# Performance work log

Measured on AMD Instinct MI355X. Metric: run time of the kernel, lower is better.

The kernel has to match this reference:

```python
import jax, jax.numpy as jnp
import numpy as np

N_P, N_A, D, H, E = 200000, 100000, 64, 32, 1000000


def setup_inputs() -> dict:
    key = jax.random.key(0)
    ks = jax.random.split(key, 32)
    inp = {}
    inp["x_paper"] = jax.random.normal(ks[0], (N_P, D), jnp.float32)
    inp["x_author"] = jax.random.normal(ks[1], (N_A, D), jnp.float32)
    inp["cites_src"] = jax.random.randint(ks[2], (E,), 0, N_P, jnp.int32)
    inp["cites_dst"] = jax.random.randint(ks[3], (E,), 0, N_P, jnp.int32)
    inp["writes_src"] = jax.random.randint(ks[4], (E,), 0, N_A, jnp.int32)
    inp["writes_dst"] = jax.random.randint(ks[5], (E,), 0, N_P, jnp.int32)
    inp["rev_src"] = jax.random.randint(ks[6], (E,), 0, N_P, jnp.int32)
    inp["rev_dst"] = jax.random.randint(ks[7], (E,), 0, N_A, jnp.int32)
    # per-relation SAGEConv params; layer 1: D->H, layer 2: H->H
    i = 8
    for layer, din in ((1, D), (2, H)):
        for rel in ("cites", "writes", "rev"):
            inp[f"W{layer}l_{rel}"] = 0.1 * jax.random.normal(ks[i], (din, H), jnp.float32); i += 1
            inp[f"W{layer}r_{rel}"] = 0.1 * jax.random.normal(ks[i], (din, H), jnp.float32); i += 1
            inp[f"b{layer}_{rel}"] = 0.01 * jax.random.normal(ks[i], (H,), jnp.float32); i += 1
    return inp


def _sage(x_src, x_dst, src, dst, Wl, Wr, b, n_dst):
    # PyG SAGEConv (aggr='mean'): lin_l(mean of source msgs) + lin_r(x_dst) + bias
    msg = x_src[src]                                              # [E, d] gather
    s = jax.ops.segment_sum(msg, dst, num_segments=n_dst)         # [n_dst, d]
    cnt = jax.ops.segment_sum(jnp.ones((src.shape[0],), x_src.dtype), dst, num_segments=n_dst)
    mean = s / jnp.maximum(cnt, 1.0)[:, None]
    return mean @ Wl + x_dst @ Wr + b


def reference(x_paper, x_author, cites_src, cites_dst, writes_src, writes_dst,
              rev_src, rev_dst,
              W1l_cites, W1r_cites, b1_cites, W1l_writes, W1r_writes, b1_writes,
              W1l_rev, W1r_rev, b1_rev,
              W2l_cites, W2r_cites, b2_cites, W2l_writes, W2r_writes, b2_writes,
              W2l_rev, W2r_rev, b2_rev):
    n_p, n_a = x_paper.shape[0], x_author.shape[0]
    # layer 1 (to_hetero sums relation outputs per dst node type), then relu
    p1 = jax.nn.relu(
        _sage(x_paper, x_paper, cites_src, cites_dst, W1l_cites, W1r_cites, b1_cites, n_p)
        + _sage(x_author, x_paper, writes_src, writes_dst, W1l_writes, W1r_writes, b1_writes, n_p))
    a1 = jax.nn.relu(
        _sage(x_paper, x_author, rev_src, rev_dst, W1l_rev, W1r_rev, b1_rev, n_a))
    # layer 2, return 'paper' output (no activation)
    p2 = (_sage(p1, p1, cites_src, cites_dst, W2l_cites, W2r_cites, b2_cites, n_p)
          + _sage(a1, p1, writes_src, writes_dst, W2l_writes, W2r_writes, b2_writes, n_p))
    return p2
```

## Files before the change

### kernel.cpp

```cpp
#include <hip/hip_runtime.h>

typedef unsigned short u16;
typedef unsigned int   u32;
typedef unsigned char  u8;
typedef __attribute__((ext_vector_type(8))) short bf16x8;
typedef __attribute__((ext_vector_type(4))) float f32x4;

#define N_P 200000
#define N_A 100000
#define DD  64
#define HH  32
#define NE  1000000
#define NBP 782
#define NBA 391
#define NB4K 245
#define NCB 196
#define P4CAP 8192
#define NB_P16 12500
#define NB_A16 6250
#define NB4K3 735

__device__ inline float bf2f(u16 u) { return __uint_as_float(((u32)u) << 16); }
__device__ inline u16 f2bf(float f) {
    u32 u = __float_as_uint(f);
    u += 0x7fffu + ((u >> 16) & 1u);
    return (u16)(u >> 16);
}
__device__ inline float lo_f(u32 m) { return __uint_as_float(m << 16); }
__device__ inline float hi_f(u32 m) { return __uint_as_float(m & 0xffff0000u); }
__device__ inline u32 cvtpk(float a, float b) {
    u32 r;
    asm("v_cvt_pk_bf16_f32 %0, %1, %2" : "=v"(r) : "v"(a), "v"(b));
    return r;
}

__device__ inline void gseg_dual(
    const u16* __restrict__ yA, const int* __restrict__ bkA, int s0, int e0,
    const u16* __restrict__ yB, const int* __restrict__ bkB, int s1, int e1,
    int lane, float& axo, float& ayo, float& bxo, float& byo) {
    float ax = 0.f, ay = 0.f, bx = 0.f, by = 0.f;
    int lastA = min(max(e0 - 1, s0), NE - 1);
    int lastB = min(max(e1 - 1, s1), NE - 1);
    for (int j0 = s0, j1 = s1; (j0 < e0) || (j1 < e1); j0 += 8, j1 += 8) {
        int ia[8], ib[8];
#pragma unroll
        for (int i = 0; i < 8; ++i) ia[i] = bkA[min(j0 + i, lastA)];
#pragma unroll
        for (int i = 0; i < 8; ++i) ib[i] = bkB[min(j1 + i, lastB)];
        u32 ma[8], mb[8];
#pragma unroll
        for (int i = 0; i < 8; ++i)
            ma[i] = *(const u32*)(yA + (size_t)(u32)ia[i] + lane * 2);
#pragma unroll
        for (int i = 0; i < 8; ++i)
            mb[i] = *(const u32*)(yB + (size_t)(u32)ib[i] + lane * 2);
#pragma unroll
        for (int i = 0; i < 8; ++i) {
            u32 va = (j0 + i < e0) ? ma[i] : 0u;
            ax += lo_f(va); ay += hi_f(va);
        }
#pragma unroll
        for (int i = 0; i < 8; ++i) {
            u32 vb = (j1 + i < e1) ? mb[i] : 0u;
            bx += lo_f(vb); by += hi_f(vb);
        }
    }
    axo = ax; ayo = ay; bxo = bx; byo = by;
}

__global__ __launch_bounds__(256) void p1_hist_k(
    const int* __restrict__ cd, const int* __restrict__ wd, const int* __restrict__ rd,
    int* __restrict__ gsizes) {
    int rel = blockIdx.y;
    const int* dst; int shift;
    if (rel == 0)      { dst = cd; shift = 10; }
    else if (rel == 1) { dst = wd; shift = 10; }
    else               { dst = rd; shift = 9;  }
    __shared__ int cnt[256];
    int t = threadIdx.x;
    cnt[t] = 0;
    __syncthreads();
    int e0 = blockIdx.x * 4096;
    if (e0 + 4096 <= NE) {
        const int4* dv = (const int4*)(dst + e0);
#pragma unroll
        for (int i = 0; i < 4; ++i) {
            int4 v = dv[i * 256 + t];
            atomicAdd(&cnt[v.x >> shift], 1);
            atomicAdd(&cnt[v.y >> shift], 1);
            atomicAdd(&cnt[v.z >> shift], 1);
            atomicAdd(&cnt[v.w >> shift], 1);
        }
    } else {
#pragma unroll
        for (int i = 0; i < 16; ++i) {
            int e = e0 + i * 256 + t;
            if (e < NE) atomicAdd(&cnt[dst[e] >> shift], 1);
        }
    }
    __syncthreads();
    if (t < NCB && cnt[t]) atomicAdd(&gsizes[rel * NCB + t], cnt[t]);
}

__global__ __launch_bounds__(256) void p2_scan_k(
    const int* __restrict__ gsizes, int* __restrict__ bases, int* __restrict__ gcur) {
    __shared__ int lds[256];
    int t = threadIdx.x;
    for (int rel = 0; rel < 3; ++rel) {
        int v = (t < NCB) ? gsizes[rel * NCB + t] : 0;
        lds[t] = v; __syncthreads();
#pragma unroll
        for (int o = 1; o < 256; o <<= 1) {
            int x = (t >= o) ? lds[t - o] : 0;
            __syncthreads();
            lds[t] += x;
            __syncthreads();
        }
        int ex = lds[t] - v;
        if (t < NCB) { bases[rel * NCB + t] = ex; gcur[rel * NCB + t] = ex; }
        __syncthreads();
    }
}

__global__ __launch_bounds__(256) void p3t1_k(
    const int* __restrict__ cs, const int* __restrict__ cd,
    const int* __restrict__ ws_, const int* __restrict__ wd,
    const int* __restrict__ rs, const int* __restrict__ rd,
    int* __restrict__ gcur,
    u32* __restrict__ pr_c, u32* __restrict__ pr_w, u32* __restrict__ pr_r,
    const float* __restrict__ xp, const float* __restrict__ xa,
    const u16* __restrict__ wt1h, const u16* __restrict__ wt1l,
    const float* __restrict__ b1s, const float* __restrict__ b1r,
    u16* __restrict__ y_pc, u16* __restrict__ y_pr, u16* __restrict__ y_aw,
    u16* __restrict__ hb_p, u16* __restrict__ hb_a) {
    __shared__ float smem[256 * 34];
    int t = threadIdx.x;
    if (blockIdx.x < NB4K3) {
        u32* sbuf  = (u32*)smem;
        int* cnt   = (int*)(smem + 4096);
        int* sc    = (int*)(smem + 4352);
        int* lcur  = (int*)(smem + 4608);
        int* gbase = (int*)(smem + 4864);
        u8*  bb    = (u8*)(smem + 5120);
        int rel = blockIdx.x / NB4K;
        int blk = blockIdx.x - rel * NB4K;
        const int *src, *dst; int shift; u32* out;
        if (rel == 0)      { src = cs;  dst = cd; shift = 10; out = pr_c; }
        else if (rel == 1) { src = ws_; dst = wd; shift = 10; out = pr_w; }
        else               { src = rs;  dst = rd; shift = 9;  out = pr_r; }
        cnt[t] = 0;
        __syncthreads();
        int e0 = blk * 4096;
        int myd[16], mys[16];
        if (e0 + 4096 <= NE) {
            const int4* dv = (const int4*)(dst + e0);
            const int4* sv = (const int4*)(src + e0);
#pragma unroll
            for (int i = 0; i < 4; ++i) {
                int4 v = dv[i * 256 + t];
                int4 s = sv[i * 256 + t];
                myd[4 * i] = v.x; myd[4 * i + 1] = v.y; myd[4 * i + 2] = v.z; myd[4 * i + 3] = v.w;
                mys[4 * i] = s.x; mys[4 * i + 1] = s.y; mys[4 * i + 2] = s.z; mys[4 * i + 3] = s.w;
                atomicAdd(&cnt[v.x >> shift], 1);
                atomicAdd(&cnt[v.y >> shift], 1);
                atomicAdd(&cnt[v.z >> shift], 1);
                atomicAdd(&cnt[v.w >> shift], 1);
            }
        } else {
#pragma unroll
            for (int i = 0; i < 4; ++i) {
#pragma unroll
                for (int c = 0; c < 4; ++c) {
                    int e = e0 + (i * 256 + t) * 4 + c;
                    int idx = 4 * i + c;
                    if (e < NE) {
                        myd[idx] = dst[e]; mys[idx] = src[e];
                        atomicAdd(&cnt[myd[idx] >> shift], 1);
                    } else { myd[idx] = -1; mys[idx] = 0; }
                }
            }
        }
        __syncthreads();
        int v = cnt[t];
        sc[t] = v; __syncthreads();
#pragma unroll
        for (int o = 1; o < 256; o <<= 1) {
            int x = (t >= o) ? sc[t - o] : 0;
            __syncthreads();
            sc[t] += x;
            __syncthreads();
        }
        int ex = sc[t] - v;
        __syncthreads();
        sc[t] = ex;
        lcur[t] = ex;
        if (t < NCB) gbase[t] = atomicAdd(&gcur[rel * NCB + t], cnt[t]);
        __syncthreads();
#pragma unroll
        for (int i = 0; i < 16; ++i) {
            if (myd[i] >= 0) {
                int d = myd[i];
                int cb = d >> shift;
                u32 dloc = (u32)(d - (cb << shift));
                u32 pk = (dloc << 18) | (u32)mys[i];
                int p = atomicAdd(&lcur[cb], 1);
                sbuf[p] = pk;
                bb[p] = (u8)cb;
            }
        }
        __syncthreads();
        int nvalid = min(4096, NE - e0);
        for (int i = t; i < nvalid; i += 256) {
            int cb = bb[i];
            out[gbase[cb] + (i - sc[cb])] = sbuf[i];
        }
    } else {
        float* Cs = smem;
        int w = t >> 6, l = t & 63;
        int lm = l & 15, lk = l >> 4;
        int bx = blockIdx.x - NB4K3;
        bool paper = bx < NBP;
        int row0 = (paper ? bx : bx - NBP) * 256;
        const float* x = paper ? xp : xa;
        int NROW = paper ? N_P : N_A;
        int nv = min(256, NROW - row0);
        bf16x8 xh[4][2], xl[4][2];
#pragma unroll
        for (int i = 0; i < 4; ++i) {
            int rowg = min(row0 + w * 64 + i * 16 + lm, NROW - 1);
            const float* rp = x + (size_t)rowg * DD + lk * 8;
#pragma unroll
            for (int kc = 0; kc < 2; ++kc) {
                float4 a = *(const float4*)(rp + kc * 32);
                float4 b = *(const float4*)(rp + kc * 32 + 4);
                float f[8] = {a.x, a.y, a.z, a.w, b.x, b.y, b.z, b.w};
                union { u32 u[4]; bf16x8 v; } H, L;
#pragma unroll
                for (int j = 0; j < 4; ++j) {
                    u32 u0 = __float_as_uint(f[2 * j]);
                    u32 u1 = __float_as_uint(f[2 * j + 1]);
                    u32 m0 = u0 & 0xffff0000u;
                    u32 m1 = u1 & 0xffff0000u;
                    H.u[j] = (u0 >> 16) | m1;
                    float l0 = f[2 * j]     - __uint_as_float(m0);
                    float l1 = f[2 * j + 1] - __uint_as_float(m1);
                    L.u[j] = cvtpk(l0, l1);
                }
                xh[i][kc] = H.v; xl[i][kc] = L.v;
            }
        }
        int nw = paper ? 3 : 2;
#pragma unroll 1
        for (int iw = 0; iw < nw; ++iw) {
            int mat = paper ? iw : (3 + iw);
            const u16* Wh = wt1h + mat * 2048;
            const u16* Wl = wt1l + mat * 2048;
            bf16x8 Bh[2][2], Bl[2][2];
#pragma unroll
            for (int ct = 0; ct < 2; ++ct)
#pragma unroll
                for (int kc = 0; kc < 2; ++kc) {
                    int off = (ct * 16 + lm) * 64 + kc * 32 + lk * 8;
                    Bh[ct][kc] = *(const bf16x8*)(Wh + off);
                    Bl[ct][kc] = *(const bf16x8*)(Wl + off);
                }
            float bv[2] = {0.f, 0.f};
            if (paper && iw == 2)  { bv[0] = b1s[lm]; bv[1] = b1s[16 + lm]; }
            if (!paper && iw == 1) { bv[0] = b1r[lm]; bv[1] = b1r[16 + lm]; }
#pragma unroll
            for (int i = 0; i < 4; ++i) {
#pragma unroll
                for (int ct = 0; ct < 2; ++ct) {
                    f32x4 acc = {bv[ct], bv[ct], bv[ct], bv[ct]};
                    acc = __builtin_amdgcn_mfma_f32_16x16x32_bf16(xh[i][0], Bh[ct][0], acc, 0, 0, 0);
                    acc = __builtin_amdgcn_mfma_f32_16x16x32_bf16(xh[i][1], Bh[ct][1], acc, 0, 0, 0);
                    acc = __builtin_amdgcn_mfma_f32_16x16x32_bf16(xl[i][0], Bh[ct][0], acc, 0, 0, 0);
                    acc = __builtin_amdgcn_mfma_f32_16x16x32_bf16(xl[i][1], Bh[ct][1], acc, 0, 0, 0);
                    acc = __builtin_amdgcn_mfma_f32_16x16x32_bf16(xh[i][0], Bl[ct][0], acc, 0, 0, 0);
                    acc = __builtin_amdgcn_mfma_f32_16x16x32_bf16(xh[i][1], Bl[ct][1], acc, 0, 0, 0);
                    int rbase = w * 64 + i * 16 + lk * 4;
#pragma unroll
                    for (int r = 0; r < 4; ++r)
                        Cs[(rbase + r) * 34 + ct * 16 + lm] = acc[r];
                }
            }
            asm volatile("s_waitcnt lgkmcnt(0)" ::: "memory");
            u16* outp;
            if (paper) outp = (iw == 0) ? y_pc : (iw == 1) ? y_pr : hb_p;
            else       outp = (iw == 0) ? y_aw : hb_a;
            u32* g = (u32*)(outp + (size_t)row0 * HH);
#pragma unroll
            for (int p = 0; p < 4; ++p) {
                int j = p * 64 + l;
                int rl = w * 64 + (j >> 2);
                if (rl < nv) {
                    const float* q = Cs + rl * 34 + (j & 3) * 8;
                    u32 o[4];
#pragma unroll
                    for (int jj = 0; jj < 4; ++jj)
                        o[jj] = cvtpk(q[2 * jj], q[2 * jj + 1]);
                    *(uint4*)(g + ((size_t)w * 256 + j) * 4) = make_uint4(o[0], o[1], o[2], o[3]);
                }
            }
            asm volatile("" ::: "memory");
        }
    }
}

__global__ __launch_bounds__(256) void p4_sort_k(
    const int* __restrict__ bases, const int* __restrict__ gsizes,
    const u32* __restrict__ pr_c, const u32* __restrict__ pr_w, const u32* __restrict__ pr_r,
    int* __restrict__ bkt_c, int* __restrict__ bkt_w, int* __restrict__ bkt_r,
    int* __restrict__ st_c, int* __restrict__ st_w, int* __restrict__ st_r) {
    int rel = blockIdx.y;
    const u32* pr; int* bkt; int* st; int width, n;
    if (rel == 0)      { pr = pr_c; bkt = bkt_c; st = st_c; width = 1024; n = N_P; }
    else if (rel == 1) { pr = pr_w; bkt = bkt_w; st = st_w; width = 1024; n = N_P; }
    else               { pr = pr_r; bkt = bkt_r; st = st_r; width = 512;  n = N_A; }
    __shared__ u32 sin[P4CAP];
    __shared__ int cnt[1024], sc2[1024], tmp[256];
    int t = threadIdx.x;
    int b = blockIdx.x;
    int base = bases[rel * NCB + b];
    int size = min(gsizes[rel * NCB + b], P4CAP);
    int d0 = b * width;
    int nd = min(width, n - d0);
    if (nd <= 0) return;
#pragma unroll
    for (int j = t; j < 1024; j += 256) cnt[j] = 0;
    __syncthreads();
    for (int i = t; i < size; i += 256) {
        u32 pk = pr[base + i];
        sin[i] = pk;
        atomicAdd(&cnt[pk >> 18], 1);
    }
    __syncthreads();
    int j0 = 4 * t;
    int c0 = cnt[j0], c1 = cnt[j0 + 1], c2 = cnt[j0 + 2], c3 = cnt[j0 + 3];
    int tot = c0 + c1 + c2 + c3;
    tmp[t] = tot; __syncthreads();
#pragma unroll
    for (int o = 1; o < 256; o <<= 1) {
        int x = (t >= o) ? tmp[t - o] : 0;
        __syncthreads();
        tmp[t] += x;
        __syncthreads();
    }
    int pre = tmp[t] - tot;
    sc2[j0] = pre;
    sc2[j0 + 1] = pre + c0;
    sc2[j0 + 2] = pre + c0 + c1;
    sc2[j0 + 3] = pre + c0 + c1 + c2;
    __syncthreads();
    for (int j = t; j < nd; j += 256) st[d0 + j] = base + sc2[j];
#pragma unroll
    for (int j = t; j < 1024; j += 256) cnt[j] = 0;
    __syncthreads();
    for (int i = t; i < size; i += 256) {
        u32 pk = sin[i];
        int dl = (int)(pk >> 18);
        int pos = sc2[dl] + atomicAdd(&cnt[dl], 1);
        bkt[base + pos] = (int)((pk & 0x3FFFFu) * HH);
    }
}

__global__ __launch_bounds__(256) void prep_w_k(
    const float* __restrict__ W1lc, const float* __restrict__ W1lr,
    const float* __restrict__ W1rc, const float* __restrict__ W1rw,
    const float* __restrict__ W1lw, const float* __restrict__ W1rr,
    const float* __restrict__ W2lc, const float* __restrict__ W2rc,
    const float* __restrict__ W2rw, const float* __restrict__ W2lw,
    const float* __restrict__ b1c, const float* __restrict__ b1w,
    const float* __restrict__ b2c, const float* __restrict__ b2w,
    u16* __restrict__ wt1h, u16* __restrict__ wt1l,
    u16* __restrict__ wt2h, u16* __restrict__ wt2l,
    float* __restrict__ b1s, float* __restrict__ b2s,
    int* __restrict__ gsizes) {
    int m = blockIdx.x, t = threadIdx.x;
    if (m == 0) {
        for (int e = t; e < 3 * NCB; e += 256) gsizes[e] = 0;
    }
    if (m < 5) {
        const float *A = nullptr, *B = nullptr;
        if (m == 0) A = W1lc;
        else if (m == 1) A = W1lr;
        else if (m == 2) { A = W1rc; B = W1rw; }
        else if (m == 3) A = W1lw;
        else A = W1rr;
        for (int e = t; e < 2048; e += 256) {
            int k = e >> 5, n = e & 31;
            float v = A[e] + (B ? B[e] : 0.f);
            u16 h = f2bf(v);
            u16 lw = f2bf(v - bf2f(h));
            wt1h[m * 2048 + n * 64 + k] = h;
            wt1l[m * 2048 + n * 64 + k] = lw;
        }
        if (m == 2 && t < HH) b1s[t] = b1c[t] + b1w[t];
    } else {
        int mm = m - 5;
        const float *A = nullptr, *B = nullptr;
        if (mm == 0) A = W2lc;
        else if (mm == 1) { A = W2rc; B = W2rw; }
        else A = W2lw;
        for (int e = t; e < 1024; e += 256) {
            int k = e >> 5, n = e & 31;
            float v = A[e] + (B ? B[e] : 0.f);
            u16 h = f2bf(v);
            u16 lw = f2bf(v - bf2f(h));
            wt2h[mm * 1024 + n * 32 + k] = h;
            wt2l[mm * 1024 + n * 32 + k] = lw;
        }
        if (mm == 1 && t < HH) b2s[t] = b2c[t] + b2w[t];
    }
}

__global__ __launch_bounds__(256) void agg1_k(
    const u16* __restrict__ y_pc, const u16* __restrict__ y_aw,
    const u16* __restrict__ y_pr,
    const int* __restrict__ st_c, const int* __restrict__ bkt_c,
    const int* __restrict__ st_w, const int* __restrict__ bkt_w,
    const int* __restrict__ st_r, const int* __restrict__ bkt_r,
    u32* __restrict__ hb_p, u32* __restrict__ hb_a) {
    int t = threadIdx.x, g = t >> 4, lane = t & 15;
    if (blockIdx.x < NB_P16) {
        int row = blockIdx.x * 16 + g;
        u32 self = hb_p[(size_t)row * (HH / 2) + lane];
        int s0 = st_c[row];
        int e0 = (row == N_P - 1) ? NE : st_c[row + 1];
        int s1 = st_w[row];
        int e1 = (row == N_P - 1) ? NE : st_w[row + 1];
        float cx, cy, wx, wy;
        gseg_dual(y_pc, bkt_c, s0, e0, y_aw, bkt_w, s1, e1, lane, cx, cy, wx, wy);
        int d0 = e0 - s0, d1 = e1 - s1;
        float iv0 = 1.0f / (float)(d0 < 1 ? 1 : d0);
        float iv1 = 1.0f / (float)(d1 < 1 ? 1 : d1);
        float ax = cx * iv0 + wx * iv1 + lo_f(self);
        float ay = cy * iv0 + wy * iv1 + hi_f(self);
        hb_p[(size_t)row * (HH / 2) + lane] = cvtpk(ax, ay);
    } else {
        int row = (blockIdx.x - NB_P16) * 16 + g;
        u32 self = hb_a[(size_t)row * (HH / 2) + lane];
        int s = st_r[row];
        int e = (row == N_A - 1) ? NE : st_r[row + 1];
        int mid = (s + e) >> 1;
        float ax0, ay0, ax1, ay1;
        gseg_dual(y_pr, bkt_r, s, mid, y_pr, bkt_r, mid, e, lane, ax0, ay0, ax1, ay1);
        int dg = e - s;
        float iv = 1.0f / (float)(dg < 1 ? 1 : dg);
        float ax = (ax0 + ax1) * iv + lo_f(self);
        float ay = (ay0 + ay1) * iv + hi_f(self);
        hb_a[(size_t)row * (HH / 2) + lane] = cvtpk(ax, ay);
    }
}

__global__ __launch_bounds__(256) void t2_k(
    const u32* __restrict__ hb_p, const u32* __restrict__ hb_a,
    const u16* __restrict__ wt2h, const u16* __restrict__ wt2l,
    const float* __restrict__ b2s,
    u16* __restrict__ z_p, u16* __restrict__ z_a, float* __restrict__ hp2) {
    __shared__ float Cs[256 * 34];
    int t = threadIdx.x, w = t >> 6, l = t & 63;
    int lm = l & 15, lk = l >> 4;
    bool paper = blockIdx.x < NBP;
    int row0 = (paper ? blockIdx.x : blockIdx.x - NBP) * 256;
    const u32* hb = paper ? hb_p : hb_a;
    int NROW = paper ? N_P : N_A;
    int nv = min(256, NROW - row0);
    bf16x8 af[4];
#pragma unroll
    for (int i = 0; i < 4; ++i) {
        int rowg = min(row0 + w * 64 + i * 16 + lm, NROW - 1);
        uint4 q = *(const uint4*)(hb + (size_t)rowg * (HH / 2) + lk * 4);
        u32 qq[4] = {q.x, q.y, q.z, q.w};
        union { u32 u[4]; bf16x8 v; } A;
#pragma unroll
        for (int j = 0; j < 4; ++j) {
            u32 m = ((qq[j] & 0x80008000u) >> 15) * 0xFFFFu;
            A.u[j] = qq[j] & ~m;
        }
        af[i] = A.v;
    }
    int nw = paper ? 2 : 1;
#pragma unroll 1
    for (int iw = 0; iw < nw; ++iw) {
        int mat = paper ? iw : 2;
        const u16* Wh = wt2h + mat * 1024;
        const u16* Wl = wt2l + mat * 1024;
        bf16x8 Bh[2], Bl[2];
#pragma unroll
        for (int ct = 0; ct < 2; ++ct) {
            int off = (ct * 16 + lm) * 32 + lk * 8;
            Bh[ct] = *(const bf16x8*)(Wh + off);
            Bl[ct] = *(const bf16x8*)(Wl + off);
        }
        float bv[2] = {0.f, 0.f};
        if (paper && iw == 1) { bv[0] = b2s[lm]; bv[1] = b2s[16 + lm]; }
#pragma unroll
        for (int i = 0; i < 4; ++i) {
#pragma unroll
            for (int ct = 0; ct < 2; ++ct) {
                f32x4 acc = {bv[ct], bv[ct], bv[ct], bv[ct]};
                acc = __builtin_amdgcn_mfma_f32_16x16x32_bf16(af[i], Bh[ct], acc, 0, 0, 0);
                acc = __builtin_amdgcn_mfma_f32_16x16x32_bf16(af[i], Bl[ct], acc, 0, 0, 0);
                int rbase = w * 64 + i * 16 + lk * 4;
#pragma unroll
                for (int r = 0; r < 4; ++r)
                    Cs[(rbase + r) * 34 + ct * 16 + lm] = acc[r];
            }
        }
        asm volatile("s_waitcnt lgkmcnt(0)" ::: "memory");
        if (paper && iw == 1) {
            float* gf = hp2 + (size_t)row0 * HH;
#pragma unroll
            for (int p = 0; p < 8; ++p) {
                int j = p * 64 + l;
                int rl = w * 64 + (j >> 3);
                if (rl < nv) {
                    const float* q = Cs + rl * 34 + (j & 7) * 4;
                    *(float4*)(gf + ((size_t)w * 512 + j) * 4) =
                        make_float4(q[0], q[1], q[2], q[3]);
                }
            }
        } else {
            u16* outp = paper ? z_p : z_a;
            u32* g = (u32*)(outp + (size_t)row0 * HH);
#pragma unroll
            for (int p = 0; p < 4; ++p) {
                int j = p * 64 + l;
                int rl = w * 64 + (j >> 2);
                if (rl < nv) {
                    const float* q = Cs + rl * 34 + (j & 3) * 8;
                    u32 o[4];
#pragma unroll
                    for (int jj = 0; jj < 4; ++jj)
                        o[jj] = cvtpk(q[2 * jj], q[2 * jj + 1]);
                    *(uint4*)(g + ((size_t)w * 256 + j) * 4) = make_uint4(o[0], o[1], o[2], o[3]);
                }
            }
        }
        asm volatile("" ::: "memory");
    }
}

__global__ __launch_bounds__(256) void agg2_k(
    const u16* __restrict__ z_p, const u16* __restrict__ z_a,
    const int* __restrict__ st_c, const int* __restrict__ bkt_c,
    const int* __restrict__ st_w, const int* __restrict__ bkt_w,
    const float* __restrict__ hp2, float* __restrict__ out) {
    int t = threadIdx.x, g = t >> 4, lane = t & 15;
    int row = blockIdx.x * 16 + g;
    float2 h = *(const float2*)(hp2 + (size_t)row * HH + lane * 2);
    int s0 = st_c[row];
    int e0 = (row == N_P - 1) ? NE : st_c[row + 1];
    int s1 = st_w[row];
    int e1 = (row == N_P - 1) ? NE : st_w[row + 1];
    float cx, cy, wx, wy;
    gseg_dual(z_p, bkt_c, s0, e0, z_a, bkt_w, s1, e1, lane, cx, cy, wx, wy);
    int d0 = e0 - s0, d1 = e1 - s1;
    float iv0 = 1.0f / (float)(d0 < 1 ? 1 : d0);
    float iv1 = 1.0f / (float)(d1 < 1 ? 1 : d1);
    float2 o = make_float2(h.x + cx * iv0 + wx * iv1,
                           h.y + cy * iv0 + wy * iv1);
    *(float2*)(out + (size_t)row * HH + lane * 2) = o;
}

extern "C" void kernel_launch(void* const* d_in, const int* in_sizes, int n_in,
                              void* d_out, int out_size, void* d_ws, size_t ws_size,
                              hipStream_t stream) {
    const float* x_p  = (const float*)d_in[0];
    const float* x_a  = (const float*)d_in[1];
    const int* c_src  = (const int*)d_in[2];
    const int* c_dst  = (const int*)d_in[3];
    const int* w_src  = (const int*)d_in[4];
    const int* w_dst  = (const int*)d_in[5];
    const int* r_src  = (const int*)d_in[6];
    const int* r_dst  = (const int*)d_in[7];
    const float* W1l_c = (const float*)d_in[8];
    const float* W1r_c = (const float*)d_in[9];
    const float* b1_c  = (const float*)d_in[10];
    const float* W1l_w = (const float*)d_in[11];
    const float* W1r_w = (const float*)d_in[12];
    const float* b1_w  = (const float*)d_in[13];
    const float* W1l_r = (const float*)d_in[14];
    const float* W1r_r = (const float*)d_in[15];
    const float* b1_r  = (const float*)d_in[16];
    const float* W2l_c = (const float*)d_in[17];
    const float* W2r_c = (const float*)d_in[18];
    const float* b2_c  = (const float*)d_in[19];
    const float* W2l_w = (const float*)d_in[20];
    const float* W2r_w = (const float*)d_in[21];
    const float* b2_w  = (const float*)d_in[22];

    int* gsizes = (int*)d_ws;
    int* bases  = gsizes + 3 * NCB;
    int* gcur   = bases + 3 * NCB;
    int* st_c   = gcur + 3 * NCB;
    int* st_w   = st_c + N_P;
    int* st_r   = st_w + N_P;
    int* bkt_c  = st_r + N_A;
    int* bkt_w  = bkt_c + NE;
    int* bkt_r  = bkt_w + NE;
    u16* wt1h  = (u16*)(bkt_r + NE);
    u16* wt1l  = wt1h + 5 * 2048;
    u16* wt2h  = wt1l + 5 * 2048;
    u16* wt2l  = wt2h + 3 * 1024;
    float* b1s = (float*)(wt2l + 3 * 1024);
    float* b2s = b1s + HH;
    u16* hb_p  = (u16*)(b2s + HH);
    u16* hb_a  = hb_p + (size_t)N_P * HH;
    u16* y_pc  = hb_a + (size_t)N_A * HH;
    u16* y_pr  = y_pc + (size_t)N_P * HH;
    u16* y_aw  = y_pr + (size_t)N_P * HH;
    float* hp2 = (float*)(y_aw + (size_t)N_A * HH);
    u32* pr_c  = (u32*)hp2;
    u32* pr_w  = pr_c + NE;
    u32* pr_r  = pr_w + NE;
    u16* z_p   = y_pc;
    u16* z_a   = y_aw;
    float* outp = (float*)d_out;

    const size_t need = ((uintptr_t)(hp2 + (size_t)N_P * HH)) - (uintptr_t)d_ws;
    if (ws_size < need) return;

    prep_w_k<<<8, 256, 0, stream>>>(W1l_c, W1l_r, W1r_c, W1r_w, W1l_w, W1r_r,
                                    W2l_c, W2r_c, W2r_w, W2l_w,
                                    b1_c, b1_w, b2_c, b2_w,
                                    wt1h, wt1l, wt2h, wt2l, b1s, b2s, gsizes);
    p1_hist_k<<<dim3(NB4K, 3), 256, 0, stream>>>(c_dst, w_dst, r_dst, gsizes);
    p2_scan_k<<<1, 256, 0, stream>>>(gsizes, bases, gcur);
    p3t1_k<<<NB4K3 + NBP + NBA, 256, 0, stream>>>(
        c_src, c_dst, w_src, w_dst, r_src, r_dst, gcur, pr_c, pr_w, pr_r,
        x_p, x_a, wt1h, wt1l, b1s, b1_r, y_pc, y_pr, y_aw, hb_p, hb_a);
    p4_sort_k<<<dim3(NCB, 3), 256, 0, stream>>>(bases, gsizes, pr_c, pr_w, pr_r,
                                                bkt_c, bkt_w, bkt_r, st_c, st_w, st_r);
    agg1_k<<<NB_P16 + NB_A16, 256, 0, stream>>>(y_pc, y_aw, y_pr,
                                                st_c, bkt_c, st_w, bkt_w, st_r, bkt_r,
                                                (u32*)hb_p, (u32*)hb_a);
    t2_k<<<NBP + NBA, 256, 0, stream>>>((const u32*)hb_p, (const u32*)hb_a,
                                        wt2h, wt2l, b2s, z_p, z_a, hp2);
    agg2_k<<<NB_P16, 256, 0, stream>>>(z_p, z_a, st_c, bkt_c, st_w, bkt_w, hp2, outp);
}
```

Baseline: 373.7 us.

## Aggregate raw layer-1 features before layer-2 transform and fuse GEMM into agg2

Drops the separate layer-2 transform kernel. Layer 2 now does mean-then-matmul: agg2 gathers the 32-wide bf16 hidden features directly, computes neighbor means, and applies Wl, Wr and the bias with per-block MFMA using hi/lo bf16 splits. The ReLU moves into agg1's store, which removes the z/hp2 intermediates and one kernel launch with its full read/write pass. In exchange, every agg2 block adds two barriers and a single-wave MFMA stage, and the gathered mean is no longer pre-rounded through a projected bf16 value.

```diff
diff --git a/kernel.cpp b/kernel.cpp
--- a/kernel.cpp
+++ b/kernel.cpp
@@ -434,8 +434,8 @@
         int d0 = e0 - s0, d1 = e1 - s1;
         float iv0 = 1.0f / (float)(d0 < 1 ? 1 : d0);
         float iv1 = 1.0f / (float)(d1 < 1 ? 1 : d1);
-        float ax = cx * iv0 + wx * iv1 + lo_f(self);
-        float ay = cy * iv0 + wy * iv1 + hi_f(self);
+        float ax = fmaxf(cx * iv0 + wx * iv1 + lo_f(self), 0.f);
+        float ay = fmaxf(cy * iv0 + wy * iv1 + hi_f(self), 0.f);
         hb_p[(size_t)row * (HH / 2) + lane] = cvtpk(ax, ay);
     } else {
         int row = (blockIdx.x - NB_P16) * 16 + g;
@@ -447,121 +447,90 @@
         gseg_dual(y_pr, bkt_r, s, mid, y_pr, bkt_r, mid, e, lane, ax0, ay0, ax1, ay1);
         int dg = e - s;
         float iv = 1.0f / (float)(dg < 1 ? 1 : dg);
-        float ax = (ax0 + ax1) * iv + lo_f(self);
-        float ay = (ay0 + ay1) * iv + hi_f(self);
+        float ax = fmaxf((ax0 + ax1) * iv + lo_f(self), 0.f);
+        float ay = fmaxf((ay0 + ay1) * iv + hi_f(self), 0.f);
         hb_a[(size_t)row * (HH / 2) + lane] = cvtpk(ax, ay);
     }
 }
 
-__global__ __launch_bounds__(256) void t2_k(
-    const u32* __restrict__ hb_p, const u32* __restrict__ hb_a,
-    const u16* __restrict__ wt2h, const u16* __restrict__ wt2l,
-    const float* __restrict__ b2s,
-    u16* __restrict__ z_p, u16* __restrict__ z_a, float* __restrict__ hp2) {
-    __shared__ float Cs[256 * 34];
-    int t = threadIdx.x, w = t >> 6, l = t & 63;
-    int lm = l & 15, lk = l >> 4;
-    bool paper = blockIdx.x < NBP;
-    int row0 = (paper ? blockIdx.x : blockIdx.x - NBP) * 256;
-    const u32* hb = paper ? hb_p : hb_a;
-    int NROW = paper ? N_P : N_A;
-    int nv = min(256, NROW - row0);
-    bf16x8 af[4];
-#pragma unroll
-    for (int i = 0; i < 4; ++i) {
-        int rowg = min(row0 + w * 64 + i * 16 + lm, NROW - 1);
-        uint4 q = *(const uint4*)(hb + (size_t)rowg * (HH / 2) + lk * 4);
-        u32 qq[4] = {q.x, q.y, q.z, q.w};
-        union { u32 u[4]; bf16x8 v; } A;
-#pragma unroll
-        for (int j = 0; j < 4; ++j) {
-            u32 m = ((qq[j] & 0x80008000u) >> 15) * 0xFFFFu;
-            A.u[j] = qq[j] & ~m;
-        }
-        af[i] = A.v;
-    }
-    int nw = paper ? 2 : 1;
-#pragma unroll 1
-    for (int iw = 0; iw < nw; ++iw) {
-        int mat = paper ? iw : 2;
-        const u16* Wh = wt2h + mat * 1024;
-        const u16* Wl = wt2l + mat * 1024;
-        bf16x8 Bh[2], Bl[2];
-#pragma unroll
-        for (int ct = 0; ct < 2; ++ct) {
-            int off = (ct * 16 + lm) * 32 + lk * 8;
-            Bh[ct] = *(const bf16x8*)(Wh + off);
-            Bl[ct] = *(const bf16x8*)(Wl + off);
-        }
-        float bv[2] = {0.f, 0.f};
-        if (paper && iw == 1) { bv[0] = b2s[lm]; bv[1] = b2s[16 + lm]; }
-#pragma unroll
-        for (int i = 0; i < 4; ++i) {
-#pragma unroll
-            for (int ct = 0; ct < 2; ++ct) {
-                f32x4 acc = {bv[ct], bv[ct], bv[ct], bv[ct]};
-                acc = __builtin_amdgcn_mfma_f32_16x16x32_bf16(af[i], Bh[ct], acc, 0, 0, 0);
-                acc = __builtin_amdgcn_mfma_f32_16x16x32_bf16(af[i], Bl[ct], acc, 0, 0, 0);
-                int rbase = w * 64 + i * 16 + lk * 4;
-#pragma unroll
-                for (int r = 0; r < 4; ++r)
-                    Cs[(rbase + r) * 34 + ct * 16 + lm] = acc[r];
-            }
-        }
-        asm volatile("s_waitcnt lgkmcnt(0)" ::: "memory");
-        if (paper && iw == 1) {
-            float* gf = hp2 + (size_t)row0 * HH;
-#pragma unroll
-            for (int p = 0; p < 8; ++p) {
-                int j = p * 64 + l;
-                int rl = w * 64 + (j >> 3);
-                if (rl < nv) {
-                    const float* q = Cs + rl * 34 + (j & 7) * 4;
-                    *(float4*)(gf + ((size_t)w * 512 + j) * 4) =
-                        make_float4(q[0], q[1], q[2], q[3]);
-                }
-            }
-        } else {
-            u16* outp = paper ? z_p : z_a;
-            u32* g = (u32*)(outp + (size_t)row0 * HH);
-#pragma unroll
-            for (int p = 0; p < 4; ++p) {
-                int j = p * 64 + l;
-                int rl = w * 64 + (j >> 2);
-                if (rl < nv) {
-                    const float* q = Cs + rl * 34 + (j & 3) * 8;
-                    u32 o[4];
-#pragma unroll
-                    for (int jj = 0; jj < 4; ++jj)
-                        o[jj] = cvtpk(q[2 * jj], q[2 * jj + 1]);
-                    *(uint4*)(g + ((size_t)w * 256 + j) * 4) = make_uint4(o[0], o[1], o[2], o[3]);
-                }
-            }
-        }
-        asm volatile("" ::: "memory");
-    }
-}
-
 __global__ __launch_bounds__(256) void agg2_k(
-    const u16* __restrict__ z_p, const u16* __restrict__ z_a,
+    const u16* __restrict__ hb_p, const u16* __restrict__ hb_a,
     const int* __restrict__ st_c, const int* __restrict__ bkt_c,
     const int* __restrict__ st_w, const int* __restrict__ bkt_w,
-    const float* __restrict__ hp2, float* __restrict__ out) {
+    const u16* __restrict__ wt2h, const u16* __restrict__ wt2l,
+    const float* __restrict__ b2s, float* __restrict__ out) {
+    __shared__ float mcs[16][34];
+    __shared__ float mws[16][34];
+    __shared__ float cso[16][34];
     int t = threadIdx.x, g = t >> 4, lane = t & 15;
-    int row = blockIdx.x * 16 + g;
-    float2 h = *(const float2*)(hp2 + (size_t)row * HH + lane * 2);
+    int row0 = blockIdx.x * 16;
+    int row = row0 + g;
     int s0 = st_c[row];
     int e0 = (row == N_P - 1) ? NE : st_c[row + 1];
     int s1 = st_w[row];
     int e1 = (row == N_P - 1) ? NE : st_w[row + 1];
     float cx, cy, wx, wy;
-    gseg_dual(z_p, bkt_c, s0, e0, z_a, bkt_w, s1, e1, lane, cx, cy, wx, wy);
+    gseg_dual(hb_p, bkt_c, s0, e0, hb_a, bkt_w, s1, e1, lane, cx, cy, wx, wy);
     int d0 = e0 - s0, d1 = e1 - s1;
     float iv0 = 1.0f / (float)(d0 < 1 ? 1 : d0);
     float iv1 = 1.0f / (float)(d1 < 1 ? 1 : d1);
-    float2 o = make_float2(h.x + cx * iv0 + wx * iv1,
-                           h.y + cy * iv0 + wy * iv1);
-    *(float2*)(out + (size_t)row * HH + lane * 2) = o;
+    mcs[g][2 * lane] = cx * iv0;  mcs[g][2 * lane + 1] = cy * iv0;
+    mws[g][2 * lane] = wx * iv1;  mws[g][2 * lane + 1] = wy * iv1;
+    __syncthreads();
+    if (t < 64) {
+        int lm = t & 15, lk = t >> 4;
+        bf16x8 as_ = *(const bf16x8*)(hb_p + (size_t)(row0 + lm) * HH + lk * 8);
+        bf16x8 mch, mcl, mwh, mwl;
+        {
+            union { u32 u[4]; bf16x8 v; } H, L;
+#pragma unroll
+            for (int j = 0; j < 4; ++j) {
+                float f0 = mcs[lm][lk * 8 + 2 * j];
+                float f1 = mcs[lm][lk * 8 + 2 * j + 1];
+                u32 u0 = __float_as_uint(f0), u1 = __float_as_uint(f1);
+                u32 m0 = u0 & 0xffff0000u, m1 = u1 & 0xffff0000u;
+                H.u[j] = (u0 >> 16) | m1;
+                L.u[j] = cvtpk(f0 - __uint_as_float(m0), f1 - __uint_as_float(m1));
+            }
+            mch = H.v; mcl = L.v;
+#pragma unroll
+            for (int j = 0; j < 4; ++j) {
+                float f0 = mws[lm][lk * 8 + 2 * j];
+                float f1 = mws[lm][lk * 8 + 2 * j + 1];
+                u32 u0 = __float_as_uint(f0), u1 = __float_as_uint(f1);
+                u32 m0 = u0 & 0xffff0000u, m1 = u1 & 0xffff0000u;
+                H.u[j] = (u0 >> 16) | m1;
+                L.u[j] = cvtpk(f0 - __uint_as_float(m0), f1 - __uint_as_float(m1));
+            }
+            mwh = H.v; mwl = L.v;
+        }
+#pragma unroll
+        for (int ct = 0; ct < 2; ++ct) {
+            int boff = (ct * 16 + lm) * 32 + lk * 8;
+            bf16x8 Bch = *(const bf16x8*)(wt2h + boff);
+            bf16x8 Bcl = *(const bf16x8*)(wt2l + boff);
+            bf16x8 Bsh = *(const bf16x8*)(wt2h + 1024 + boff);
+            bf16x8 Bsl = *(const bf16x8*)(wt2l + 1024 + boff);
+            bf16x8 Bwh = *(const bf16x8*)(wt2h + 2048 + boff);
+            bf16x8 Bwl = *(const bf16x8*)(wt2l + 2048 + boff);
+            float bb = b2s[ct * 16 + lm];
+            f32x4 acc = {bb, bb, bb, bb};
+            acc = __builtin_amdgcn_mfma_f32_16x16x32_bf16(as_, Bsh, acc, 0, 0, 0);
+            acc = __builtin_amdgcn_mfma_f32_16x16x32_bf16(as_, Bsl, acc, 0, 0, 0);
+            acc = __builtin_amdgcn_mfma_f32_16x16x32_bf16(mch, Bch, acc, 0, 0, 0);
+            acc = __builtin_amdgcn_mfma_f32_16x16x32_bf16(mcl, Bch, acc, 0, 0, 0);
+            acc = __builtin_amdgcn_mfma_f32_16x16x32_bf16(mch, Bcl, acc, 0, 0, 0);
+            acc = __builtin_amdgcn_mfma_f32_16x16x32_bf16(mwh, Bwh, acc, 0, 0, 0);
+            acc = __builtin_amdgcn_mfma_f32_16x16x32_bf16(mwl, Bwh, acc, 0, 0, 0);
+            acc = __builtin_amdgcn_mfma_f32_16x16x32_bf16(mwh, Bwl, acc, 0, 0, 0);
+#pragma unroll
+            for (int r = 0; r < 4; ++r)
+                cso[lk * 4 + r][ct * 16 + lm] = acc[r];
+        }
+    }
+    __syncthreads();
+    int r = t >> 4, c = (t & 15) * 2;
+    *(float2*)(out + (size_t)(row0 + r) * HH + c) = make_float2(cso[r][c], cso[r][c + 1]);
 }
 
 extern "C" void kernel_launch(void* const* d_in, const int* in_sizes, int n_in,
@@ -611,15 +580,13 @@
     u16* y_pc  = hb_a + (size_t)N_A * HH;
     u16* y_pr  = y_pc + (size_t)N_P * HH;
     u16* y_aw  = y_pr + (size_t)N_P * HH;
-    float* hp2 = (float*)(y_aw + (size_t)N_A * HH);
-    u32* pr_c  = (u32*)hp2;
+    float* tail = (float*)(y_aw + (size_t)N_A * HH);
+    u32* pr_c  = (u32*)tail;
     u32* pr_w  = pr_c + NE;
     u32* pr_r  = pr_w + NE;
-    u16* z_p   = y_pc;
-    u16* z_a   = y_aw;
     float* outp = (float*)d_out;
 
-    const size_t need = ((uintptr_t)(hp2 + (size_t)N_P * HH)) - (uintptr_t)d_ws;
+    const size_t need = ((uintptr_t)(pr_r + NE)) - (uintptr_t)d_ws;
     if (ws_size < need) return;
 
     prep_w_k<<<8, 256, 0, stream>>>(W1l_c, W1l_r, W1r_c, W1r_w, W1l_w, W1r_r,
@@ -636,7 +603,6 @@
     agg1_k<<<NB_P16 + NB_A16, 256, 0, stream>>>(y_pc, y_aw, y_pr,
                                                 st_c, bkt_c, st_w, bkt_w, st_r, bkt_r,
                                                 (u32*)hb_p, (u32*)hb_a);
-    t2_k<<<NBP + NBA, 256, 0, stream>>>((const u32*)hb_p, (const u32*)hb_a,
-                                        wt2h, wt2l, b2s, z_p, z_a, hp2);
-    agg2_k<<<NB_P16, 256, 0, stream>>>(z_p, z_a, st_c, bkt_c, st_w, bkt_w, hp2, outp);
-}
+    agg2_k<<<NB_P16, 256, 0, stream>>>(hb_p, hb_a, st_c, bkt_c, st_w, bkt_w,
+                                       wt2h, wt2l, b2s, outp);
+}
```

New measurement: 363.6 us. -2.7%, faster.
